# Optimization experiments

Hardware: AMD Instinct MI355X
Metric: run time of the kernel (lower is better)

Reference implementation:

```python
import jax, jax.numpy as jnp
import numpy as np

B, S, D = 1, 2048, 2048
H, HKV = 16, 4
HD = D // H  # 128
E, TOPK, F = 8, 2, 2048
CLIP = 8.0
THETA = 500000.0
EPS = 1e-5


def setup_inputs() -> dict:
    key = jax.random.key(0)
    ks = jax.random.split(key, 12)
    s = lambda k, shape, scale: jax.random.normal(k, shape, dtype=jnp.float32) * scale
    return {
        "hidden_states": s(ks[0], (B, S, D), 1.0),
        "position_ids": jnp.broadcast_to(jnp.arange(S, dtype=jnp.int32), (B, S)),
        "ln1_w": jnp.ones((D,), jnp.float32),
        "ln1_b": jnp.zeros((D,), jnp.float32),
        "ln2_w": jnp.ones((D,), jnp.float32),
        "ln2_b": jnp.zeros((D,), jnp.float32),
        "Wqkv": s(ks[1], (D, (H + 2 * HKV) * HD), 0.02),
        "Wout": s(ks[2], (D, D), 0.02),
        "Wrouter": s(ks[3], (D, E), 0.02),
        "w1": s(ks[4], (E, D, F), 0.02),
        "v1": s(ks[5], (E, D, F), 0.02),
        "w2": s(ks[6], (E, F, D), 0.02),
    }


def _layernorm(x, w, b):
    mu = jnp.mean(x, axis=-1, keepdims=True)
    var = jnp.mean((x - mu) ** 2, axis=-1, keepdims=True)
    return (x - mu) * jax.lax.rsqrt(var + EPS) * w + b


def _rope(x, pos):
    # x: [B,S,h,HD], neox style (rotate halves)
    half = HD // 2
    inv_freq = 1.0 / (THETA ** (jnp.arange(0, HD, 2, dtype=jnp.float32) / HD))
    ang = pos.astype(jnp.float32)[..., None] * inv_freq  # [B,S,half]
    cos = jnp.cos(ang)[:, :, None, :]
    sin = jnp.sin(ang)[:, :, None, :]
    x1, x2 = x[..., :half], x[..., half:]
    return jnp.concatenate([x1 * cos - x2 * sin, x2 * cos + x1 * sin], axis=-1)


def _forward(hidden_states, position_ids, ln1_w, ln1_b, ln2_w, ln2_b,
             Wqkv, Wout, Wrouter, w1, v1, w2):
    residual = hidden_states
    h = _layernorm(hidden_states, ln1_w, ln1_b)
    qkv = jnp.clip(h @ Wqkv, -CLIP, CLIP)
    q, k, v = jnp.split(qkv, [H * HD, H * HD + HKV * HD], axis=-1)
    q = q.reshape(B, S, H, HD)
    k = k.reshape(B, S, HKV, HD)
    v = v.reshape(B, S, HKV, HD)
    q = _rope(q, position_ids)
    k = _rope(k, position_ids)
    # GQA: repeat kv heads
    rep = H // HKV
    k = jnp.repeat(k, rep, axis=2)
    v = jnp.repeat(v, rep, axis=2)
    scale = HD ** -0.5
    scores = jnp.einsum("bqhd,bkhd->bhqk", q, k) * scale
    causal = jnp.tril(jnp.ones((S, S), dtype=bool))
    scores = jnp.where(causal, scores, jnp.float32(-1e9))
    probs = jax.nn.softmax(scores, axis=-1)
    attn = jnp.einsum("bhqk,bkhd->bqhd", probs, v).reshape(B, S, D)
    attn = attn @ Wout
    h = residual + attn
    residual = h
    h = _layernorm(h, ln2_w, ln2_b)

    # MoE over flattened tokens
    x = h.reshape(-1, D)  # [T,D]
    logits = x @ Wrouter  # [T,E]
    rw = jax.nn.softmax(logits.astype(jnp.float32), axis=-1)
    top_w, top_idx = jax.lax.top_k(rw, TOPK)  # [T,TOPK]
    top_w = top_w / jnp.sum(top_w, axis=-1, keepdims=True)
    acc = jnp.zeros_like(x)
    for e in range(E):  # fixed small expert count, matches source structure
        ew = jnp.sum(top_w * (top_idx == e), axis=-1, keepdims=True)  # [T,1]
        inter = jax.nn.silu(x @ w1[e]) * (x @ v1[e])
        acc = acc + (inter @ w2[e]) * ew
    out = acc.reshape(B, S, D) + residual
    return out


def reference(hidden_states, position_ids, ln1_w, ln1_b, ln2_w, ln2_b,
              Wqkv, Wout, Wrouter, w1, v1, w2):
    return _forward(hidden_states, position_ids, ln1_w, ln1_b, ln2_w, ln2_b,
                    Wqkv, Wout, Wrouter, w1, v1, w2)
```

## Files before the change

kernel.cpp:

```cpp
#include <hip/hip_runtime.h>
#include <cstdint>
#include <cstddef>
#include <cmath>

typedef unsigned short u16;
typedef unsigned int u32;
typedef __attribute__((ext_vector_type(8))) _Float16 f16x8;
typedef __attribute__((ext_vector_type(4))) float f32x4;

#define S_LEN 2048
#define DMODEL 2048
#define NHEAD 16
#define NKVH 4
#define HDIM 128
#define NQKV 3072
#define NF 2048
#define TA 4096
#define ATT_SCALE 0.08838834764831845f
#define LO_SCALE 1024.0f
#define LO_INV (1.0f/1024.0f)
#define DEFER_THR 8.0f

static __device__ __forceinline__ u16 f2h(float x){ _Float16 h=(_Float16)x; return __builtin_bit_cast(u16,h); }
static __device__ __forceinline__ float h2f(u16 u){ return (float)__builtin_bit_cast(_Float16,u); }
static __device__ __forceinline__ void split2(float x, u16& hi, u16& lo){
  hi = f2h(x);
  lo = f2h((x - h2f(hi)) * LO_SCALE);
}
static __device__ __forceinline__ void gload16(const u16* g, u16* l){
  __builtin_amdgcn_global_load_lds(
      (const __attribute__((address_space(1))) void*)g,
      (__attribute__((address_space(3))) void*)l, 16, 0, 0);
}
static __device__ __forceinline__ void xcd_swz(int& bx, int& by){
  int gx = gridDim.x;
  int n = gx * gridDim.y;
  int bid = by*gx + bx;
  int cpx = n >> 3;
  int s = (bid & 7)*cpx + (bid >> 3);
  bx = s % gx; by = s / gx;
}

#define WS_WOUTH ((size_t)0)
#define WS_WOUTL ((size_t)8388608)
#define WS_QKVTH ((size_t)16777216)
#define WS_QKVTL ((size_t)29360128)
#define WS_H1H   ((size_t)41943040)
#define WS_H1L   ((size_t)50331648)
#define WS_QKV   ((size_t)58720256)
#define WS_QH    ((size_t)16777216)
#define WS_QL    ((size_t)25165824)
#define WS_KH    ((size_t)33554432)
#define WS_KL    ((size_t)35651584)
#define WS_VTH   ((size_t)37748736)
#define WS_VTL   ((size_t)39845888)
#define WS_OH    ((size_t)41943040)
#define WS_OL    ((size_t)50331648)
#define WS_H2    ((size_t)58720256)
#define WS_X2    ((size_t)75497472)
#define WS_I1    ((size_t)0)
#define WS_Y     ((size_t)16777216)
#define WS_MOE   ((size_t)33554432)
#define WS_SM    ((size_t)83886080)
#define WS_WT    ((size_t)84934656)
#define SM_INVT   0
#define SM_COUNTS 256
#define SM_FILL   320
#define SM_OFFS   384
#define SM_NT     448
#define SM_TE     512
#define SM_TRS    768
#define SM_E01    1024
#define SM_W01    (1024+16384)
#define SM_ATOK   (1024+2*16384)
#define SM_AW     (1024+3*16384)
#define SM_SLOT   (1024+4*16384)

__global__ void __launch_bounds__(64) init_k(int* counts, int* fill, float* invt){
  int t = threadIdx.x;
  if (t < 8) { counts[t] = 0; fill[t] = 0; }
  double di = (double)t * (1.0/64.0);
  float y = (float)pow(500000.0, di);
  invt[t] = 1.0f / y;
}

__global__ void __launch_bounds__(256) wsplit_k(const float* __restrict__ W,
    u16* __restrict__ Th, u16* __restrict__ Tl, int N){
  __shared__ float tile[32][33];
  int n0 = blockIdx.x*32, k0 = blockIdx.y*32;
  int tid = threadIdx.x;
  int rr = tid >> 3, cg = tid & 7;
  #pragma unroll
  for (int j=0;j<4;++j)
    tile[rr][cg*4+j] = W[(size_t)(k0+rr)*N + n0 + cg*4 + j];
  __syncthreads();
  int cc = tid >> 3, sg = tid & 7;
  #pragma unroll
  for (int j=0;j<4;++j){
    float x = tile[sg*4+j][cc];
    u16 hi, lo; split2(x, hi, lo);
    size_t idx = (size_t)(n0+cc)*2048 + k0 + sg*4 + j;
    Th[idx] = hi; Tl[idx] = lo;
  }
}

__global__ void __launch_bounds__(256) wconvT_k(const float* __restrict__ W,
                                                u16* __restrict__ T){
  __shared__ float tile[64][68];
  int n0 = blockIdx.x*64, k0 = blockIdx.y*64;
  size_t ebase = (size_t)blockIdx.z * 2048 * 2048;
  int tid = threadIdx.x;
  int rr = tid >> 4, c4 = (tid & 15)*4;
  #pragma unroll
  for (int p=0;p<4;++p){
    float4 v = *(const float4*)(W + ebase + (size_t)(k0+p*16+rr)*2048 + n0 + c4);
    *(float4*)&tile[p*16+rr][c4] = v;
  }
  __syncthreads();
  int nn = tid >> 2, kc = (tid & 3)*16;
  u16 buf[16];
  #pragma unroll
  for (int j=0;j<16;++j) buf[j] = f2h(tile[kc+j][nn]);
  u16* dst = T + ebase + (size_t)(n0+nn)*2048 + k0 + kc;
  *(int4*)dst = *(int4*)&buf[0];
  *(int4*)(dst+8) = *(int4*)&buf[8];
}

__device__ __forceinline__ float blk_red_sum(float v, float* red, int tid){
  #pragma unroll
  for (int off=1; off<64; off<<=1) v += __shfl_xor(v, off);
  if ((tid&63)==0) red[tid>>6] = v;
  __syncthreads();
  float r = red[0]+red[1]+red[2]+red[3];
  __syncthreads();
  return r;
}

__global__ void __launch_bounds__(256) ln1_k(const float* __restrict__ X,
    const float* __restrict__ W, const float* __restrict__ Bv,
    u16* __restrict__ Hh, u16* __restrict__ Hl){
  __shared__ float red[4];
  int t = blockIdx.x, tid = threadIdx.x;
  const float* row = X + (size_t)t*DMODEL + tid*8;
  float4 a = *(const float4*)row;
  float4 b = *(const float4*)(row+4);
  float xs[8] = {a.x,a.y,a.z,a.w,b.x,b.y,b.z,b.w};
  float s = 0.f;
  #pragma unroll
  for (int j=0;j<8;++j) s += xs[j];
  float mu = blk_red_sum(s, red, tid) * (1.f/DMODEL);
  float sq = 0.f;
  #pragma unroll
  for (int j=0;j<8;++j){ float d = xs[j]-mu; sq += d*d; }
  float var = blk_red_sum(sq, red, tid) * (1.f/DMODEL);
  float rs = 1.0f/sqrtf(var + 1e-5f);
  float4 w0 = *(const float4*)(W + tid*8);
  float4 w1 = *(const float4*)(W + tid*8 + 4);
  float4 b0 = *(const float4*)(Bv + tid*8);
  float4 b1 = *(const float4*)(Bv + tid*8 + 4);
  float ws_[8] = {w0.x,w0.y,w0.z,w0.w,w1.x,w1.y,w1.z,w1.w};
  float bs_[8] = {b0.x,b0.y,b0.z,b0.w,b1.x,b1.y,b1.z,b1.w};
  u32 ph[4], pl[4];
  #pragma unroll
  for (int j=0;j<4;++j){
    u16 h0,l0,h1,l1;
    split2((xs[2*j]-mu)*rs*ws_[2*j]+bs_[2*j], h0, l0);
    split2((xs[2*j+1]-mu)*rs*ws_[2*j+1]+bs_[2*j+1], h1, l1);
    ph[j] = (u32)h0 | ((u32)h1<<16);
    pl[j] = (u32)l0 | ((u32)l1<<16);
  }
  int4 vh; vh.x=(int)ph[0]; vh.y=(int)ph[1]; vh.z=(int)ph[2]; vh.w=(int)ph[3];
  int4 vl; vl.x=(int)pl[0]; vl.y=(int)pl[1]; vl.z=(int)pl[2]; vl.w=(int)pl[3];
  *(int4*)(Hh + (size_t)t*DMODEL + tid*8) = vh;
  *(int4*)(Hl + (size_t)t*DMODEL + tid*8) = vl;
}

template<int MODE>
__global__ void __launch_bounds__(256) gemm32_k(
    const u16* __restrict__ Ahp, const u16* __restrict__ Alp,
    const u16* __restrict__ Bhp, const u16* __restrict__ Blp,
    float* __restrict__ C, const float* __restrict__ res)
{
  constexpr int K = 2048;
  __shared__ u16 Ash[128*32], Asl[128*32], Bsh[128*32], Bsl[128*32];
  int bx = blockIdx.x, by = blockIdx.y;
  xcd_swz(bx, by);
  int m0 = by*128, n0 = bx*128;
  int tid = threadIdx.x, w = tid>>6, lane = tid&63;
  int l15 = lane&15, l4 = lane>>4, wr = w>>1, wc = w&1;
  int srow = lane>>2;
  int scol = ((lane&3) ^ ((lane>>3)&3))*8;

  f32x4 accH[4][4] = {}, accC[4][4] = {};

  for (int k0 = 0; k0 < K; k0 += 32){
    __syncthreads();
    #pragma unroll
    for (int c=0;c<2;++c){
      int row = w*32 + c*16 + srow;
      size_t ga = (size_t)(m0+row)*K + k0 + scol;
      size_t gb = (size_t)(n0+row)*K + k0 + scol;
      gload16(Ahp+ga, &Ash[(w*32+c*16)*32]);
      gload16(Alp+ga, &Asl[(w*32+c*16)*32]);
      gload16(Bhp+gb, &Bsh[(w*32+c*16)*32]);
      gload16(Blp+gb, &Bsl[(w*32+c*16)*32]);
    }
    __syncthreads();
    int fsl = (l4 ^ ((l15>>1)&3))*8;
    f16x8 ah[4], al[4];
    #pragma unroll
    for (int mi=0; mi<4; ++mi){
      int row = wr*64 + mi*16 + l15;
      ah[mi] = *(const f16x8*)&Ash[row*32 + fsl];
      al[mi] = *(const f16x8*)&Asl[row*32 + fsl];
    }
    #pragma unroll
    for (int ni=0; ni<4; ++ni){
      int row = wc*64 + ni*16 + l15;
      f16x8 bh = *(const f16x8*)&Bsh[row*32 + fsl];
      f16x8 bl = *(const f16x8*)&Bsl[row*32 + fsl];
      #pragma unroll
      for (int mi=0; mi<4; ++mi){
        accH[mi][ni] = __builtin_amdgcn_mfma_f32_16x16x32_f16(ah[mi], bh, accH[mi][ni], 0,0,0);
        accC[mi][ni] = __builtin_amdgcn_mfma_f32_16x16x32_f16(ah[mi], bl, accC[mi][ni], 0,0,0);
        accC[mi][ni] = __builtin_amdgcn_mfma_f32_16x16x32_f16(al[mi], bh, accC[mi][ni], 0,0,0);
      }
    }
  }

  #pragma unroll
  for (int mi=0; mi<4; ++mi){
    #pragma unroll
    for (int ni=0; ni<4; ++ni){
      #pragma unroll
      for (int r=0; r<4; ++r){
        int rl = wr*64 + mi*16 + l4*4 + r;
        int cl = wc*64 + ni*16 + l15;
        float v = accH[mi][ni][r] + accC[mi][ni][r]*LO_INV;
        if constexpr (MODE == 0){
          v = fminf(fmaxf(v, -8.f), 8.f);
          C[(size_t)(m0 + rl)*NQKV + n0 + cl] = v;
        } else {
          size_t idx = (size_t)(m0 + rl)*DMODEL + n0 + cl;
          C[idx] = v + res[idx];
        }
      }
    }
  }
}

__global__ void __launch_bounds__(256) rope_k(const float* __restrict__ qkv,
    const int* __restrict__ pos_ids, const float* __restrict__ invt,
    u16* __restrict__ Qh, u16* __restrict__ Ql, u16* __restrict__ Kh, u16* __restrict__ Kl){
  int s = blockIdx.x;
  float pos = (float)pos_ids[s];
  const float* row = qkv + (size_t)s*NQKV;
  for (int p = threadIdx.x; p < 1280; p += 256){
    int i = p & 63;
    float ang = pos * invt[i];
    float sn, cs;
    sincosf(ang, &sn, &cs);
    u16 h1_,l1_,h2_,l2_;
    if (p < 1024){
      int h = p >> 6;
      float x1 = row[h*HDIM + i];
      float x2 = row[h*HDIM + 64 + i];
      size_t base = ((size_t)h*S_LEN + s)*HDIM;
      split2(x1*cs - x2*sn, h1_, l1_);
      split2(x2*cs + x1*sn, h2_, l2_);
      Qh[base + i] = h1_; Ql[base + i] = l1_;
      Qh[base + 64 + i] = h2_; Ql[base + 64 + i] = l2_;
    } else {
      int kh = (p-1024) >> 6;
      float x1 = row[2048 + kh*HDIM + i];
      float x2 = row[2048 + kh*HDIM + 64 + i];
      size_t base = ((size_t)kh*S_LEN + s)*HDIM;
      split2(x1*cs - x2*sn, h1_, l1_);
      split2(x2*cs + x1*sn, h2_, l2_);
      Kh[base + i] = h1_; Kl[base + i] = l1_;
      Kh[base + 64 + i] = h2_; Kl[base + 64 + i] = l2_;
    }
  }
}

__global__ void __launch_bounds__(256) vtrans_k(const float* __restrict__ qkv,
    u16* __restrict__ Vth, u16* __restrict__ Vtl){
  __shared__ float tile[32][33];
  int s0 = blockIdx.x*32, c0 = blockIdx.y*32;
  int tid = threadIdx.x;
  int rr = tid >> 3, cg = tid & 7;
  #pragma unroll
  for (int j=0;j<4;++j)
    tile[rr][cg*4+j] = qkv[(size_t)(s0+rr)*NQKV + 2560 + c0 + cg*4 + j];
  __syncthreads();
  int cc = tid >> 3, sg = tid & 7;
  #pragma unroll
  for (int j=0;j<4;++j){
    float x = tile[sg*4+j][cc];
    u16 hi, lo; split2(x, hi, lo);
    size_t idx = (size_t)(c0+cc)*S_LEN + s0 + sg*4 + j;
    Vth[idx] = hi; Vtl[idx] = lo;
  }
}

__global__ void __launch_bounds__(256) attn_k(
    const u16* __restrict__ Qhp, const u16* __restrict__ Qlp,
    const u16* __restrict__ Khp, const u16* __restrict__ Klp,
    const u16* __restrict__ Vthp, const u16* __restrict__ Vtlp,
    u16* __restrict__ Oh, u16* __restrict__ Ol){
  __shared__ u16 Ksh[32*128], Ksl[32*128];
  __shared__ u16 Vsh[128*32], Vsl[128*32];
  __shared__ u16 Psh[4*16*40], Psl[4*16*40];
  int tid = threadIdx.x;
  int w = tid>>6, lane = tid&63, l15 = lane&15, l4 = lane>>4;
  int qb = 31 - blockIdx.x;
  int h = blockIdx.y, kvh = h>>2;
  int q0 = qb*64 + w*16;
  f16x8 qfh[4], qfl[4];
  #pragma unroll
  for (int ds=0; ds<4; ++ds){
    size_t off = ((size_t)h*S_LEN + q0 + l15)*HDIM + ds*32 + l4*8;
    qfh[ds] = *(const f16x8*)(Qhp + off);
    qfl[ds] = *(const f16x8*)(Qlp + off);
  }
  f32x4 accH[8] = {}, accC[8] = {};
  float m_r[4], l_r[4];
  #pragma unroll
  for (int r=0;r<4;++r){ m_r[r] = -1e30f; l_r[r] = 0.f; }
  int ntile = 2*qb + 2;
  for (int kb = 0; kb < ntile; ++kb){
    int kbase = kb*32;
    __syncthreads();
    #pragma unroll
    for (int c=0;c<2;++c){
      int krow = w*8 + c*4 + (lane>>4);
      int ks = lane&15;
      int kcol = ((ks&8) | ((ks&7) ^ (krow&7)))*8;
      size_t koff = ((size_t)kvh*S_LEN + kbase + krow)*HDIM + kcol;
      gload16(Khp + koff, &Ksh[(w*8+c*4)*128]);
      gload16(Klp + koff, &Ksl[(w*8+c*4)*128]);
      int vrow = w*32 + c*16 + (lane>>2);
      int vcol = (((lane&3) ^ ((lane>>3)&3)))*8;
      size_t voff = ((size_t)kvh*HDIM + vrow)*S_LEN + kbase + vcol;
      gload16(Vthp + voff, &Vsh[(w*32+c*16)*32]);
      gload16(Vtlp + voff, &Vsl[(w*32+c*16)*32]);
    }
    __syncthreads();
    f32x4 sH0 = {}, sH1 = {}, sC0 = {}, sC1 = {};
    #pragma unroll
    for (int ds=0; ds<4; ++ds){
      int ksl = ds*4 + l4;
      int klds = ((ksl&8) | ((ksl&7) ^ (l15&7)))*8;
      f16x8 kh0 = *(const f16x8*)&Ksh[l15*128 + klds];
      f16x8 kl0 = *(const f16x8*)&Ksl[l15*128 + klds];
      f16x8 kh1 = *(const f16x8*)&Ksh[(16+l15)*128 + klds];
      f16x8 kl1 = *(const f16x8*)&Ksl[(16+l15)*128 + klds];
      sH0 = __builtin_amdgcn_mfma_f32_16x16x32_f16(qfh[ds], kh0, sH0, 0,0,0);
      sC0 = __builtin_amdgcn_mfma_f32_16x16x32_f16(qfh[ds], kl0, sC0, 0,0,0);
      sC0 = __builtin_amdgcn_mfma_f32_16x16x32_f16(qfl[ds], kh0, sC0, 0,0,0);
      sH1 = __builtin_amdgcn_mfma_f32_16x16x32_f16(qfh[ds], kh1, sH1, 0,0,0);
      sC1 = __builtin_amdgcn_mfma_f32_16x16x32_f16(qfh[ds], kl1, sC1, 0,0,0);
      sC1 = __builtin_amdgcn_mfma_f32_16x16x32_f16(qfl[ds], kh1, sC1, 0,0,0);
    }
    float v0[4], v1[4];
    bool need = false;
    #pragma unroll
    for (int r=0;r<4;++r){
      int qg = q0 + l4*4 + r;
      v0[r] = (sH0[r] + sC0[r]*LO_INV)*ATT_SCALE; if (kbase + l15 > qg) v0[r] = -1e9f;
      v1[r] = (sH1[r] + sC1[r]*LO_INV)*ATT_SCALE; if (kbase + 16 + l15 > qg) v1[r] = -1e9f;
      float pm = fmaxf(v0[r], v1[r]);
      need = need || (pm > m_r[r] + DEFER_THR);
    }
    if (__any(need)){
      float fac[4];
      #pragma unroll
      for (int r=0;r<4;++r){
        float mx = fmaxf(v0[r], v1[r]);
        mx = fmaxf(mx, __shfl_xor(mx,1));
        mx = fmaxf(mx, __shfl_xor(mx,2));
        mx = fmaxf(mx, __shfl_xor(mx,4));
        mx = fmaxf(mx, __shfl_xor(mx,8));
        float mnew = fmaxf(m_r[r], mx);
        fac[r] = __expf(m_r[r] - mnew);
        l_r[r] *= fac[r];
        m_r[r] = mnew;
      }
      #pragma unroll
      for (int nt=0; nt<8; ++nt){
        #pragma unroll
        for (int r=0;r<4;++r){ accH[nt][r] *= fac[r]; accC[nt][r] *= fac[r]; }
      }
    }
    #pragma unroll
    for (int r=0;r<4;++r){
      float p0 = __expf(v0[r] - m_r[r]);
      float p1 = __expf(v1[r] - m_r[r]);
      l_r[r] += p0 + p1;
      u16 hi, lo;
      split2(p0, hi, lo);
      Psh[w*640 + (l4*4+r)*40 + l15] = hi;
      Psl[w*640 + (l4*4+r)*40 + l15] = lo;
      split2(p1, hi, lo);
      Psh[w*640 + (l4*4+r)*40 + 16 + l15] = hi;
      Psl[w*640 + (l4*4+r)*40 + 16 + l15] = lo;
    }
    f16x8 pfh = *(const f16x8*)&Psh[w*640 + l15*40 + l4*8];
    f16x8 pfl = *(const f16x8*)&Psl[w*640 + l15*40 + l4*8];
    #pragma unroll
    for (int nt=0; nt<8; ++nt){
      int vsl = (l4 ^ ((l15>>1)&3))*8;
      f16x8 vh = *(const f16x8*)&Vsh[(nt*16 + l15)*32 + vsl];
      f16x8 vl = *(const f16x8*)&Vsl[(nt*16 + l15)*32 + vsl];
      accH[nt] = __builtin_amdgcn_mfma_f32_16x16x32_f16(pfh, vh, accH[nt], 0,0,0);
      f32x4 aC = __builtin_amdgcn_mfma_f32_16x16x32_f16(pfh, vl, accC[nt], 0,0,0);
      accC[nt] = __builtin_amdgcn_mfma_f32_16x16x32_f16(pfl, vh, aC, 0,0,0);
    }
  }
  #pragma unroll
  for (int r=0;r<4;++r){
    float l = l_r[r];
    l += __shfl_xor(l,1); l += __shfl_xor(l,2);
    l += __shfl_xor(l,4); l += __shfl_xor(l,8);
    l_r[r] = l;
  }
  #pragma unroll
  for (int nt=0; nt<8; ++nt){
    #pragma unroll
    for (int r=0;r<4;++r){
      int row = q0 + l4*4 + r;
      int col = h*HDIM + nt*16 + l15;
      float val = (accH[nt][r] + accC[nt][r]*LO_INV) / l_r[r];
      u16 hi, lo; split2(val, hi, lo);
      Oh[(size_t)row*DMODEL + col] = hi;
      Ol[(size_t)row*DMODEL + col] = lo;
    }
  }
}

__global__ void __launch_bounds__(256) ln2_router_k(const float* __restrict__ H2,
    const float* __restrict__ W, const float* __restrict__ Bv,
    const float* __restrict__ Wr, u16* __restrict__ X2,
    int* __restrict__ e01, float* __restrict__ w01, int* __restrict__ counts){
  __shared__ float red[4];
  __shared__ float lred[4][8];
  int t = blockIdx.x, tid = threadIdx.x;
  const float* row = H2 + (size_t)t*DMODEL + tid*8;
  float4 a = *(const float4*)row;
  float4 b = *(const float4*)(row+4);
  float xs[8] = {a.x,a.y,a.z,a.w,b.x,b.y,b.z,b.w};
  float s = 0.f;
  #pragma unroll
  for (int j=0;j<8;++j) s += xs[j];
  float mu = blk_red_sum(s, red, tid) * (1.f/DMODEL);
  float sq = 0.f;
  #pragma unroll
  for (int j=0;j<8;++j){ float d = xs[j]-mu; sq += d*d; }
  float var = blk_red_sum(sq, red, tid) * (1.f/DMODEL);
  float rs = 1.0f/sqrtf(var + 1e-5f);
  float4 w0 = *(const float4*)(W + tid*8);
  float4 w1 = *(const float4*)(W + tid*8 + 4);
  float4 b0 = *(const float4*)(Bv + tid*8);
  float4 b1 = *(const float4*)(Bv + tid*8 + 4);
  float ws_[8] = {w0.x,w0.y,w0.z,w0.w,w1.x,w1.y,w1.z,w1.w};
  float bs_[8] = {b0.x,b0.y,b0.z,b0.w,b1.x,b1.y,b1.z,b1.w};
  float xn[8];
  #pragma unroll
  for (int j=0;j<8;++j) xn[j] = (xs[j]-mu)*rs*ws_[j]+bs_[j];
  u32 pk[4];
  #pragma unroll
  for (int j=0;j<4;++j) pk[j] = (u32)f2h(xn[2*j]) | ((u32)f2h(xn[2*j+1])<<16);
  int4 v; v.x=(int)pk[0]; v.y=(int)pk[1]; v.z=(int)pk[2]; v.w=(int)pk[3];
  *(int4*)(X2 + (size_t)t*DMODEL + tid*8) = v;
  float lg[8] = {0,0,0,0,0,0,0,0};
  #pragma unroll
  for (int j=0;j<8;++j){
    const float* wrp = Wr + (size_t)(tid*8 + j)*8;
    float4 wa = *(const float4*)wrp;
    float4 wb = *(const float4*)(wrp+4);
    lg[0]+=xn[j]*wa.x; lg[1]+=xn[j]*wa.y; lg[2]+=xn[j]*wa.z; lg[3]+=xn[j]*wa.w;
    lg[4]+=xn[j]*wb.x; lg[5]+=xn[j]*wb.y; lg[6]+=xn[j]*wb.z; lg[7]+=xn[j]*wb.w;
  }
  #pragma unroll
  for (int e=0;e<8;++e){
    #pragma unroll
    for (int off=1; off<64; off<<=1) lg[e] += __shfl_xor(lg[e], off);
  }
  if ((tid&63)==0){
    #pragma unroll
    for (int e=0;e<8;++e) lred[tid>>6][e] = lg[e];
  }
  __syncthreads();
  if (tid==0){
    float L[8];
    #pragma unroll
    for (int e=0;e<8;++e) L[e] = lred[0][e]+lred[1][e]+lred[2][e]+lred[3][e];
    int e0 = 0;
    #pragma unroll
    for (int e=1;e<8;++e) if (L[e] > L[e0]) e0 = e;
    int e1 = (e0==0)?1:0;
    #pragma unroll
    for (int e=0;e<8;++e) if (e!=e0 && L[e] > L[e1]) e1 = e;
    float ax = expf(L[e1]-L[e0]);
    float z = 1.f/(1.f+ax);
    e01[2*t] = e0; e01[2*t+1] = e1;
    w01[2*t] = z;  w01[2*t+1] = ax*z;
    atomicAdd(&counts[e0],1); atomicAdd(&counts[e1],1);
  }
}

__global__ void __launch_bounds__(64) htiles_k(const int* counts, int* offs, int* ntl,
                                               int* te, int* trs){
  if (threadIdx.x==0){
    int off=0;
    for (int e=0;e<8;++e){ offs[e]=off; off+=counts[e]; }
    offs[8]=off;
    int nt=0;
    for (int e=0;e<8;++e)
      for (int j=0; j*128 < counts[e]; ++j){ te[nt]=e; trs[nt]=j*128; nt++; }
    ntl[0]=nt;
  }
}

__global__ void __launch_bounds__(256) scatter_k(const int* __restrict__ e01,
    const float* __restrict__ w01, const int* __restrict__ offs, int* __restrict__ fill,
    int* __restrict__ atok, float* __restrict__ aw, int* __restrict__ slots){
  int t = blockIdx.x*256 + threadIdx.x;
  if (t >= S_LEN) return;
  int e0 = e01[2*t], e1 = e01[2*t+1];
  int p0 = offs[e0] + atomicAdd(&fill[e0],1);
  atok[p0] = t; aw[p0] = w01[2*t]; slots[2*t] = p0;
  int p1 = offs[e1] + atomicAdd(&fill[e1],1);
  atok[p1] = t; aw[p1] = w01[2*t+1]; slots[2*t+1] = p1;
}

template<int MODE>
__global__ void __launch_bounds__(256) gemm_moe_k(
    const u16* __restrict__ A, const u16* __restrict__ BT, void* __restrict__ C,
    const u16* __restrict__ i1g, const float* __restrict__ aw,
    const int* __restrict__ atok, const int* __restrict__ counts,
    const int* __restrict__ offs, const int* __restrict__ ntl,
    const int* __restrict__ te, const int* __restrict__ trs)
{
  constexpr int K = 2048;
  __shared__ u16 As[128*32], Bs[128*32];
  int bx = blockIdx.x, by = blockIdx.y;
  xcd_swz(bx, by);
  if (by >= ntl[0]) return;
  int e = te[by];
  int rsu = trs[by];
  int base = offs[e] + rsu;
  int valid = min(128, counts[e] - rsu);
  const u16* Bp = BT + (size_t)e * 2048 * 2048;
  int tid = threadIdx.x, w = tid>>6, lane = tid&63;
  int l15 = lane & 15, l4 = lane >> 4;
  int wr = w >> 1, wc = w & 1;
  int srow = lane>>2;
  int scol = ((lane&3) ^ ((lane>>3)&3))*8;
  int n0 = bx*128;
  int tokc[2];
  #pragma unroll
  for (int c=0;c<2;++c){
    int rr = w*32 + c*16 + srow;
    if constexpr (MODE == 2 || MODE == 3)
      tokc[c] = atok[min(base + rr, TA-1)] & (S_LEN-1);
    else
      tokc[c] = min(base + rr, TA-1);
  }

  f32x4 acc[4][4] = {};

  for (int k0 = 0; k0 < K; k0 += 32){
    __syncthreads();
    #pragma unroll
    for (int c=0;c<2;++c){
      gload16(A + (size_t)tokc[c]*K + k0 + scol, &As[(w*32+c*16)*32]);
      int row = w*32 + c*16 + srow;
      gload16(Bp + (size_t)(n0+row)*K + k0 + scol, &Bs[(w*32+c*16)*32]);
    }
    __syncthreads();
    int fsl = (l4 ^ ((l15>>1)&3))*8;
    f16x8 af[4];
    #pragma unroll
    for (int mi=0; mi<4; ++mi)
      af[mi] = *(const f16x8*)&As[(wr*64 + mi*16 + l15)*32 + fsl];
    #pragma unroll
    for (int ni=0; ni<4; ++ni){
      f16x8 bfv = *(const f16x8*)&Bs[(wc*64 + ni*16 + l15)*32 + fsl];
      #pragma unroll
      for (int mi=0; mi<4; ++mi)
        acc[mi][ni] = __builtin_amdgcn_mfma_f32_16x16x32_f16(af[mi], bfv, acc[mi][ni], 0,0,0);
    }
  }

  #pragma unroll
  for (int mi=0; mi<4; ++mi){
    #pragma unroll
    for (int ni=0; ni<4; ++ni){
      f32x4 v = acc[mi][ni];
      #pragma unroll
      for (int r=0; r<4; ++r){
        int rl = wr*64 + mi*16 + l4*4 + r;
        int cl = wc*64 + ni*16 + l15;
        int col = n0 + cl;
        if (rl >= valid) continue;
        if constexpr (MODE == 2){
          ((u16*)C)[(size_t)(base + rl)*NF + col] = f2h(v[r]);
        } else if constexpr (MODE == 3){
          size_t idx = (size_t)(base + rl)*NF + col;
          float a = h2f(i1g[idx]);
          float sl = a / (1.f + __expf(-a));
          ((u16*)C)[idx] = f2h(sl * v[r]);
        } else {
          float wgt = aw[base + rl];
          ((u16*)C)[(size_t)(base + rl)*DMODEL + col] = f2h(v[r] * wgt);
        }
      }
    }
  }
}

__global__ void __launch_bounds__(256) combine_k(const float* __restrict__ H2,
    const u16* __restrict__ MOE, const int* __restrict__ slots, float* __restrict__ out){
  int t = blockIdx.x, tid = threadIdx.x;
  int s0 = slots[2*t], s1 = slots[2*t+1];
  const float* h2p = H2 + (size_t)t*DMODEL + tid*8;
  int4 b0 = *(const int4*)(MOE + (size_t)s0*DMODEL + tid*8);
  int4 b1 = *(const int4*)(MOE + (size_t)s1*DMODEL + tid*8);
  const u16* bp0 = (const u16*)&b0;
  const u16* bp1 = (const u16*)&b1;
  float* op = out + (size_t)t*DMODEL + tid*8;
  #pragma unroll
  for (int j=0;j<8;++j)
    op[j] = h2p[j] + h2f(bp0[j]) + h2f(bp1[j]);
}

extern "C" void kernel_launch(void* const* d_in, const int* in_sizes, int n_in,
                              void* d_out, int out_size, void* d_ws, size_t ws_size,
                              hipStream_t stream){
  const float* hidden = (const float*)d_in[0];
  const int*   pos    = (const int*)d_in[1];
  const float* ln1w   = (const float*)d_in[2];
  const float* ln1b   = (const float*)d_in[3];
  const float* ln2w   = (const float*)d_in[4];
  const float* ln2b   = (const float*)d_in[5];
  const float* Wqkv   = (const float*)d_in[6];
  const float* Wout   = (const float*)d_in[7];
  const float* Wr     = (const float*)d_in[8];
  const float* w1     = (const float*)d_in[9];
  const float* v1     = (const float*)d_in[10];
  const float* w2     = (const float*)d_in[11];
  float* out = (float*)d_out;
  char* ws = (char*)d_ws;

  u16* woutTh = (u16*)(ws + WS_WOUTH);
  u16* woutTl = (u16*)(ws + WS_WOUTL);
  u16* qkvTh  = (u16*)(ws + WS_QKVTH);
  u16* qkvTl  = (u16*)(ws + WS_QKVTL);
  u16* h1h = (u16*)(ws + WS_H1H);
  u16* h1l = (u16*)(ws + WS_H1L);
  float* qkv = (float*)(ws + WS_QKV);
  u16* Qh = (u16*)(ws + WS_QH);
  u16* Ql = (u16*)(ws + WS_QL);
  u16* Kh = (u16*)(ws + WS_KH);
  u16* Kl = (u16*)(ws + WS_KL);
  u16* Vth = (u16*)(ws + WS_VTH);
  u16* Vtl = (u16*)(ws + WS_VTL);
  u16* Oh = (u16*)(ws + WS_OH);
  u16* Ol = (u16*)(ws + WS_OL);
  float* h2 = (float*)(ws + WS_H2);
  u16* x2 = (u16*)(ws + WS_X2);
  u16* i1 = (u16*)(ws + WS_I1);
  u16* Yb = (u16*)(ws + WS_Y);
  u16* moe = (u16*)(ws + WS_MOE);
  u16* wT = (u16*)(ws + WS_WT);
  char* sm = ws + WS_SM;
  float* invt = (float*)(sm + SM_INVT);
  int* counts = (int*)(sm + SM_COUNTS);
  int* fill   = (int*)(sm + SM_FILL);
  int* offs   = (int*)(sm + SM_OFFS);
  int* ntl    = (int*)(sm + SM_NT);
  int* te     = (int*)(sm + SM_TE);
  int* trs    = (int*)(sm + SM_TRS);
  int* e01    = (int*)(sm + SM_E01);
  float* w01  = (float*)(sm + SM_W01);
  int* atok   = (int*)(sm + SM_ATOK);
  float* aw   = (float*)(sm + SM_AW);
  int* slots  = (int*)(sm + SM_SLOT);

  init_k<<<1, 64, 0, stream>>>(counts, fill, invt);
  wsplit_k<<<dim3(96,64), 256, 0, stream>>>(Wqkv, qkvTh, qkvTl, NQKV);
  wsplit_k<<<dim3(64,64), 256, 0, stream>>>(Wout, woutTh, woutTl, DMODEL);
  ln1_k<<<S_LEN, 256, 0, stream>>>(hidden, ln1w, ln1b, h1h, h1l);
  gemm32_k<0><<<dim3(24,16), 256, 0, stream>>>(h1h, h1l, qkvTh, qkvTl, qkv, nullptr);
  rope_k<<<S_LEN, 256, 0, stream>>>(qkv, pos, invt, Qh, Ql, Kh, Kl);
  vtrans_k<<<dim3(64,16), 256, 0, stream>>>(qkv, Vth, Vtl);
  attn_k<<<dim3(32,16), 256, 0, stream>>>(Qh, Ql, Kh, Kl, Vth, Vtl, Oh, Ol);
  gemm32_k<1><<<dim3(16,16), 256, 0, stream>>>(Oh, Ol, woutTh, woutTl, h2, hidden);
  ln2_router_k<<<S_LEN, 256, 0, stream>>>(h2, ln2w, ln2b, Wr, x2, e01, w01, counts);
  htiles_k<<<1, 64, 0, stream>>>(counts, offs, ntl, te, trs);
  scatter_k<<<8, 256, 0, stream>>>(e01, w01, offs, fill, atok, aw, slots);
  wconvT_k<<<dim3(32,32,8), 256, 0, stream>>>(w1, wT);
  gemm_moe_k<2><<<dim3(16,40), 256, 0, stream>>>(x2, wT, i1, nullptr, nullptr,
      atok, counts, offs, ntl, te, trs);
  wconvT_k<<<dim3(32,32,8), 256, 0, stream>>>(v1, wT);
  gemm_moe_k<3><<<dim3(16,40), 256, 0, stream>>>(x2, wT, Yb, i1, nullptr,
      atok, counts, offs, ntl, te, trs);
  wconvT_k<<<dim3(32,32,8), 256, 0, stream>>>(w2, wT);
  gemm_moe_k<4><<<dim3(16,40), 256, 0, stream>>>(Yb, wT, moe, nullptr, aw,
      atok, counts, offs, ntl, te, trs);
  combine_k<<<S_LEN, 256, 0, stream>>>(h2, moe, slots, out);
}
```

Baseline: 837.1 us.

## Fuse MoE gate/up GEMMs with SiLU epilogue and halve GEMM N-tiles

Adds a fused MoE kernel that computes the x@w1 and x@v1 products together, sharing the A tile and applying SiLU(a)*b in the epilogue. This removes the fp16 intermediate i1 write and re-read and one full pass over the gathered activations. It needs a second transposed-weight buffer, so it is only used when the workspace is large enough; otherwise the old three-step path runs. Separately, all GEMMs drop from 128x128 to 128x64 output tiles with twice the grid size, giving more blocks to fill the CUs but more A-tile reloads.

```diff
diff --git a/kernel.cpp b/kernel.cpp
--- a/kernel.cpp
+++ b/kernel.cpp
@@ -62,7 +62,9 @@
 #define WS_Y     ((size_t)16777216)
 #define WS_MOE   ((size_t)33554432)
 #define WS_SM    ((size_t)83886080)
-#define WS_WT    ((size_t)84934656)
+#define WS_WT0   ((size_t)84934656)
+#define WS_WT1   ((size_t)152043520)
+#define WS_BIG   ((size_t)219152384)
 #define SM_INVT   0
 #define SM_COUNTS 256
 #define SM_FILL   320
@@ -182,16 +184,16 @@
     float* __restrict__ C, const float* __restrict__ res)
 {
   constexpr int K = 2048;
-  __shared__ u16 Ash[128*32], Asl[128*32], Bsh[128*32], Bsl[128*32];
+  __shared__ u16 Ash[128*32], Asl[128*32], Bsh[64*32], Bsl[64*32];
   int bx = blockIdx.x, by = blockIdx.y;
   xcd_swz(bx, by);
-  int m0 = by*128, n0 = bx*128;
+  int m0 = by*128, n0 = bx*64;
   int tid = threadIdx.x, w = tid>>6, lane = tid&63;
   int l15 = lane&15, l4 = lane>>4, wr = w>>1, wc = w&1;
   int srow = lane>>2;
   int scol = ((lane&3) ^ ((lane>>3)&3))*8;
 
-  f32x4 accH[4][4] = {}, accC[4][4] = {};
+  f32x4 accH[4][2] = {}, accC[4][2] = {};
 
   for (int k0 = 0; k0 < K; k0 += 32){
     __syncthreads();
@@ -199,11 +201,14 @@
     for (int c=0;c<2;++c){
       int row = w*32 + c*16 + srow;
       size_t ga = (size_t)(m0+row)*K + k0 + scol;
-      size_t gb = (size_t)(n0+row)*K + k0 + scol;
       gload16(Ahp+ga, &Ash[(w*32+c*16)*32]);
       gload16(Alp+ga, &Asl[(w*32+c*16)*32]);
-      gload16(Bhp+gb, &Bsh[(w*32+c*16)*32]);
-      gload16(Blp+gb, &Bsl[(w*32+c*16)*32]);
+    }
+    {
+      int rowb = w*16 + srow;
+      size_t gb = (size_t)(n0+rowb)*K + k0 + scol;
+      gload16(Bhp+gb, &Bsh[(w*16)*32]);
+      gload16(Blp+gb, &Bsl[(w*16)*32]);
     }
     __syncthreads();
     int fsl = (l4 ^ ((l15>>1)&3))*8;
@@ -215,8 +220,8 @@
       al[mi] = *(const f16x8*)&Asl[row*32 + fsl];
     }
     #pragma unroll
-    for (int ni=0; ni<4; ++ni){
-      int row = wc*64 + ni*16 + l15;
+    for (int ni=0; ni<2; ++ni){
+      int row = wc*32 + ni*16 + l15;
       f16x8 bh = *(const f16x8*)&Bsh[row*32 + fsl];
       f16x8 bl = *(const f16x8*)&Bsl[row*32 + fsl];
       #pragma unroll
@@ -231,11 +236,11 @@
   #pragma unroll
   for (int mi=0; mi<4; ++mi){
     #pragma unroll
-    for (int ni=0; ni<4; ++ni){
+    for (int ni=0; ni<2; ++ni){
       #pragma unroll
       for (int r=0; r<4; ++r){
         int rl = wr*64 + mi*16 + l4*4 + r;
-        int cl = wc*64 + ni*16 + l15;
+        int cl = wc*32 + ni*16 + l15;
         float v = accH[mi][ni][r] + accC[mi][ni][r]*LO_INV;
         if constexpr (MODE == 0){
           v = fminf(fmaxf(v, -8.f), 8.f);
@@ -534,6 +539,86 @@
   atok[p1] = t; aw[p1] = w01[2*t+1]; slots[2*t+1] = p1;
 }
 
+__global__ void __launch_bounds__(256) gemm_moe13_k(
+    const u16* __restrict__ A, const u16* __restrict__ B1T, const u16* __restrict__ B2T,
+    u16* __restrict__ Y,
+    const int* __restrict__ atok, const int* __restrict__ counts,
+    const int* __restrict__ offs, const int* __restrict__ ntl,
+    const int* __restrict__ te, const int* __restrict__ trs)
+{
+  constexpr int K = 2048;
+  __shared__ u16 As[128*32], B1s[64*32], B2s[64*32];
+  int bx = blockIdx.x, by = blockIdx.y;
+  xcd_swz(bx, by);
+  if (by >= ntl[0]) return;
+  int e = te[by];
+  int rsu = trs[by];
+  int base = offs[e] + rsu;
+  int valid = min(128, counts[e] - rsu);
+  const u16* B1p = B1T + (size_t)e * 2048 * 2048;
+  const u16* B2p = B2T + (size_t)e * 2048 * 2048;
+  int tid = threadIdx.x, w = tid>>6, lane = tid&63;
+  int l15 = lane & 15, l4 = lane >> 4;
+  int wr = w >> 1, wc = w & 1;
+  int srow = lane>>2;
+  int scol = ((lane&3) ^ ((lane>>3)&3))*8;
+  int n0 = bx*64;
+  int tokc[2];
+  #pragma unroll
+  for (int c=0;c<2;++c){
+    int rr = w*32 + c*16 + srow;
+    tokc[c] = atok[min(base + rr, TA-1)] & (S_LEN-1);
+  }
+
+  f32x4 acc1[4][2] = {}, acc2[4][2] = {};
+
+  for (int k0 = 0; k0 < K; k0 += 32){
+    __syncthreads();
+    #pragma unroll
+    for (int c=0;c<2;++c)
+      gload16(A + (size_t)tokc[c]*K + k0 + scol, &As[(w*32+c*16)*32]);
+    {
+      int rowb = w*16 + srow;
+      size_t gb = (size_t)(n0+rowb)*K + k0 + scol;
+      gload16(B1p + gb, &B1s[(w*16)*32]);
+      gload16(B2p + gb, &B2s[(w*16)*32]);
+    }
+    __syncthreads();
+    int fsl = (l4 ^ ((l15>>1)&3))*8;
+    f16x8 af[4];
+    #pragma unroll
+    for (int mi=0; mi<4; ++mi)
+      af[mi] = *(const f16x8*)&As[(wr*64 + mi*16 + l15)*32 + fsl];
+    #pragma unroll
+    for (int ni=0; ni<2; ++ni){
+      int row = wc*32 + ni*16 + l15;
+      f16x8 b1 = *(const f16x8*)&B1s[row*32 + fsl];
+      f16x8 b2 = *(const f16x8*)&B2s[row*32 + fsl];
+      #pragma unroll
+      for (int mi=0; mi<4; ++mi){
+        acc1[mi][ni] = __builtin_amdgcn_mfma_f32_16x16x32_f16(af[mi], b1, acc1[mi][ni], 0,0,0);
+        acc2[mi][ni] = __builtin_amdgcn_mfma_f32_16x16x32_f16(af[mi], b2, acc2[mi][ni], 0,0,0);
+      }
+    }
+  }
+
+  #pragma unroll
+  for (int mi=0; mi<4; ++mi){
+    #pragma unroll
+    for (int ni=0; ni<2; ++ni){
+      #pragma unroll
+      for (int r=0; r<4; ++r){
+        int rl = wr*64 + mi*16 + l4*4 + r;
+        if (rl >= valid) continue;
+        int col = n0 + wc*32 + ni*16 + l15;
+        float a = acc1[mi][ni][r];
+        float sl = a / (1.f + __expf(-a));
+        Y[(size_t)(base + rl)*NF + col] = f2h(sl * acc2[mi][ni][r]);
+      }
+    }
+  }
+}
+
 template<int MODE>
 __global__ void __launch_bounds__(256) gemm_moe_k(
     const u16* __restrict__ A, const u16* __restrict__ BT, void* __restrict__ C,
@@ -543,7 +628,7 @@
     const int* __restrict__ te, const int* __restrict__ trs)
 {
   constexpr int K = 2048;
-  __shared__ u16 As[128*32], Bs[128*32];
+  __shared__ u16 As[128*32], Bs[64*32];
   int bx = blockIdx.x, by = blockIdx.y;
   xcd_swz(bx, by);
   if (by >= ntl[0]) return;
@@ -557,7 +642,7 @@
   int wr = w >> 1, wc = w & 1;
   int srow = lane>>2;
   int scol = ((lane&3) ^ ((lane>>3)&3))*8;
-  int n0 = bx*128;
+  int n0 = bx*64;
   int tokc[2];
   #pragma unroll
   for (int c=0;c<2;++c){
@@ -568,15 +653,16 @@
       tokc[c] = min(base + rr, TA-1);
   }
 
-  f32x4 acc[4][4] = {};
+  f32x4 acc[4][2] = {};
 
   for (int k0 = 0; k0 < K; k0 += 32){
     __syncthreads();
     #pragma unroll
-    for (int c=0;c<2;++c){
+    for (int c=0;c<2;++c)
       gload16(A + (size_t)tokc[c]*K + k0 + scol, &As[(w*32+c*16)*32]);
-      int row = w*32 + c*16 + srow;
-      gload16(Bp + (size_t)(n0+row)*K + k0 + scol, &Bs[(w*32+c*16)*32]);
+    {
+      int rowb = w*16 + srow;
+      gload16(Bp + (size_t)(n0+rowb)*K + k0 + scol, &Bs[(w*16)*32]);
     }
     __syncthreads();
     int fsl = (l4 ^ ((l15>>1)&3))*8;
@@ -585,8 +671,8 @@
     for (int mi=0; mi<4; ++mi)
       af[mi] = *(const f16x8*)&As[(wr*64 + mi*16 + l15)*32 + fsl];
     #pragma unroll
-    for (int ni=0; ni<4; ++ni){
-      f16x8 bfv = *(const f16x8*)&Bs[(wc*64 + ni*16 + l15)*32 + fsl];
+    for (int ni=0; ni<2; ++ni){
+      f16x8 bfv = *(const f16x8*)&Bs[(wc*32 + ni*16 + l15)*32 + fsl];
       #pragma unroll
       for (int mi=0; mi<4; ++mi)
         acc[mi][ni] = __builtin_amdgcn_mfma_f32_16x16x32_f16(af[mi], bfv, acc[mi][ni], 0,0,0);
@@ -596,14 +682,13 @@
   #pragma unroll
   for (int mi=0; mi<4; ++mi){
     #pragma unroll
-    for (int ni=0; ni<4; ++ni){
+    for (int ni=0; ni<2; ++ni){
       f32x4 v = acc[mi][ni];
       #pragma unroll
       for (int r=0; r<4; ++r){
         int rl = wr*64 + mi*16 + l4*4 + r;
-        int cl = wc*64 + ni*16 + l15;
-        int col = n0 + cl;
         if (rl >= valid) continue;
+        int col = n0 + wc*32 + ni*16 + l15;
         if constexpr (MODE == 2){
           ((u16*)C)[(size_t)(base + rl)*NF + col] = f2h(v[r]);
         } else if constexpr (MODE == 3){
@@ -673,7 +758,8 @@
   u16* i1 = (u16*)(ws + WS_I1);
   u16* Yb = (u16*)(ws + WS_Y);
   u16* moe = (u16*)(ws + WS_MOE);
-  u16* wT = (u16*)(ws + WS_WT);
+  u16* wT0 = (u16*)(ws + WS_WT0);
+  u16* wT1 = (u16*)(ws + WS_WT1);
   char* sm = ws + WS_SM;
   float* invt = (float*)(sm + SM_INVT);
   int* counts = (int*)(sm + SM_COUNTS);
@@ -692,22 +778,32 @@
   wsplit_k<<<dim3(96,64), 256, 0, stream>>>(Wqkv, qkvTh, qkvTl, NQKV);
   wsplit_k<<<dim3(64,64), 256, 0, stream>>>(Wout, woutTh, woutTl, DMODEL);
   ln1_k<<<S_LEN, 256, 0, stream>>>(hidden, ln1w, ln1b, h1h, h1l);
-  gemm32_k<0><<<dim3(24,16), 256, 0, stream>>>(h1h, h1l, qkvTh, qkvTl, qkv, nullptr);
+  gemm32_k<0><<<dim3(48,16), 256, 0, stream>>>(h1h, h1l, qkvTh, qkvTl, qkv, nullptr);
   rope_k<<<S_LEN, 256, 0, stream>>>(qkv, pos, invt, Qh, Ql, Kh, Kl);
   vtrans_k<<<dim3(64,16), 256, 0, stream>>>(qkv, Vth, Vtl);
   attn_k<<<dim3(32,16), 256, 0, stream>>>(Qh, Ql, Kh, Kl, Vth, Vtl, Oh, Ol);
-  gemm32_k<1><<<dim3(16,16), 256, 0, stream>>>(Oh, Ol, woutTh, woutTl, h2, hidden);
+  gemm32_k<1><<<dim3(32,16), 256, 0, stream>>>(Oh, Ol, woutTh, woutTl, h2, hidden);
   ln2_router_k<<<S_LEN, 256, 0, stream>>>(h2, ln2w, ln2b, Wr, x2, e01, w01, counts);
   htiles_k<<<1, 64, 0, stream>>>(counts, offs, ntl, te, trs);
   scatter_k<<<8, 256, 0, stream>>>(e01, w01, offs, fill, atok, aw, slots);
-  wconvT_k<<<dim3(32,32,8), 256, 0, stream>>>(w1, wT);
-  gemm_moe_k<2><<<dim3(16,40), 256, 0, stream>>>(x2, wT, i1, nullptr, nullptr,
-      atok, counts, offs, ntl, te, trs);
-  wconvT_k<<<dim3(32,32,8), 256, 0, stream>>>(v1, wT);
-  gemm_moe_k<3><<<dim3(16,40), 256, 0, stream>>>(x2, wT, Yb, i1, nullptr,
-      atok, counts, offs, ntl, te, trs);
-  wconvT_k<<<dim3(32,32,8), 256, 0, stream>>>(w2, wT);
-  gemm_moe_k<4><<<dim3(16,40), 256, 0, stream>>>(Yb, wT, moe, nullptr, aw,
-      atok, counts, offs, ntl, te, trs);
+  if (ws_size >= WS_BIG){
+    wconvT_k<<<dim3(32,32,8), 256, 0, stream>>>(w1, wT0);
+    wconvT_k<<<dim3(32,32,8), 256, 0, stream>>>(v1, wT1);
+    gemm_moe13_k<<<dim3(32,40), 256, 0, stream>>>(x2, wT0, wT1, Yb,
+        atok, counts, offs, ntl, te, trs);
+    wconvT_k<<<dim3(32,32,8), 256, 0, stream>>>(w2, wT0);
+    gemm_moe_k<4><<<dim3(32,40), 256, 0, stream>>>(Yb, wT0, moe, nullptr, aw,
+        atok, counts, offs, ntl, te, trs);
+  } else {
+    wconvT_k<<<dim3(32,32,8), 256, 0, stream>>>(w1, wT0);
+    gemm_moe_k<2><<<dim3(32,40), 256, 0, stream>>>(x2, wT0, i1, nullptr, nullptr,
+        atok, counts, offs, ntl, te, trs);
+    wconvT_k<<<dim3(32,32,8), 256, 0, stream>>>(v1, wT0);
+    gemm_moe_k<3><<<dim3(32,40), 256, 0, stream>>>(x2, wT0, Yb, i1, nullptr,
+        atok, counts, offs, ntl, te, trs);
+    wconvT_k<<<dim3(32,32,8), 256, 0, stream>>>(w2, wT0);
+    gemm_moe_k<4><<<dim3(32,40), 256, 0, stream>>>(Yb, wT0, moe, nullptr, aw,
+        atok, counts, offs, ntl, te, trs);
+  }
   combine_k<<<S_LEN, 256, 0, stream>>>(h2, moe, slots, out);
 }
```

Measured after the change: 791.5 us. 5.4% less time.
